# Optimization experiments

Hardware: AMD Instinct MI355X
Metric: run time of the kernel (lower is better)

The kernel has to match this reference:

```python
import jax, jax.numpy as jnp
import numpy as np

EPS = 1e-5
HEADS, K, U, M = 4, 16, 1, 11


def _bn(z, gamma, beta, mean, var):
    # z: [b, c, n]; BN in eval mode (running stats)
    inv = jax.lax.rsqrt(var + EPS)
    return (z - mean[None, :, None]) * (gamma * inv)[None, :, None] + beta[None, :, None]


def setup_inputs() -> dict:
    key = jax.random.key(0)
    ks = jax.random.split(key, 16)
    b, C, w, h = 8, 256, 64, 64
    vv = 256 // HEADS  # out_channels // heads = 64
    inp = {}
    inp['x'] = jax.random.normal(ks[0], (b, C, w, h), dtype=jnp.float32)
    sc = 1.0 / np.sqrt(C)
    inp['Wq'] = jax.random.normal(ks[1], (K * HEADS, C), dtype=jnp.float32) * sc
    inp['q_gamma'] = jnp.ones((K * HEADS,), jnp.float32)
    inp['q_beta'] = jnp.zeros((K * HEADS,), jnp.float32)
    inp['q_mean'] = jax.random.normal(ks[2], (K * HEADS,), dtype=jnp.float32) * 0.1
    inp['q_var'] = jax.random.uniform(ks[3], (K * HEADS,), minval=0.5, maxval=1.5, dtype=jnp.float32)
    inp['Wk'] = jax.random.normal(ks[4], (K * U, C), dtype=jnp.float32) * sc
    inp['Wv'] = jax.random.normal(ks[5], (vv * U, C), dtype=jnp.float32) * sc
    inp['v_gamma'] = jnp.ones((vv * U,), jnp.float32)
    inp['v_beta'] = jnp.zeros((vv * U,), jnp.float32)
    inp['v_mean'] = jax.random.normal(ks[6], (vv * U,), dtype=jnp.float32) * 0.1
    inp['v_var'] = jax.random.uniform(ks[7], (vv * U,), minval=0.5, maxval=1.5, dtype=jnp.float32)
    inp['embedding'] = jax.random.normal(ks[8], (K, U, 1, M, M), dtype=jnp.float32)
    return inp


def reference(x, Wq, q_gamma, q_beta, q_mean, q_var, Wk, Wv,
              v_gamma, v_beta, v_mean, v_var, embedding):
    b, C, w, h = x.shape
    n = w * h
    vv = Wv.shape[0] // U
    xf = x.reshape(b, C, n)

    # queries: 1x1 conv + BN -> [b, heads, k, n]
    q = _bn(jnp.einsum('oc,bcn->bon', Wq, xf), q_gamma, q_beta, q_mean, q_var)
    q = q.reshape(b, HEADS, K, n)

    # keys: 1x1 conv, softmax over spatial positions -> [b, k, u, n]
    keys = jnp.einsum('oc,bcn->bon', Wk, xf).reshape(b, K, U, n)
    sm = jax.nn.softmax(keys, axis=-1)

    # values: 1x1 conv + BN -> [b, vv, u, n]
    values = _bn(jnp.einsum('oc,bcn->bon', Wv, xf), v_gamma, v_beta, v_mean, v_var)
    values = values.reshape(b, vv, U, n)

    # content lambda
    lam_c = jnp.einsum('bkun,bvun->bkv', sm, values)          # [b, k, vv]
    y_c = jnp.einsum('bhkn,bkv->bhvn', q, lam_c)              # [b, h, vv, n]

    # position lambda via conv3d over (vv, w, h) with kernel (1, m, m)
    v5 = values.reshape(b, U, vv, w, h)                       # torch .view reinterpret
    pad = (M - 1) // 2
    lam_p = jax.lax.conv_general_dilated(
        v5, embedding, window_strides=(1, 1, 1),
        padding=((0, 0), (pad, pad), (pad, pad)),
        dimension_numbers=('NCDHW', 'OIDHW', 'NCDHW'))        # [b, k, vv, w, h]
    lam_p = lam_p.reshape(b, K, vv, n)
    y_p = jnp.einsum('bhkn,bkvn->bhvn', q, lam_p)             # [b, h, vv, n]

    out = (y_c + y_p).reshape(b, HEADS * vv, w, h)
    return out
```

## Files before the change

kernel.cpp:

```cpp
#include <hip/hip_runtime.h>
#include <math.h>

#define EPSBN 1e-5f

constexpr int B_ = 8, C_ = 256, N_ = 4096, IMG_ = 64;
constexpr int HEADS_ = 4, K_ = 16, VV_ = 64, M_ = 11, OC_ = 144;

typedef _Float16 half4 __attribute__((ext_vector_type(4)));
typedef _Float16 half8 __attribute__((ext_vector_type(8)));
typedef __fp16 fp16x2 __attribute__((ext_vector_type(2)));
typedef float f32x4 __attribute__((ext_vector_type(4)));

constexpr size_t O_WT   = 0;
constexpr size_t O_BIAS = 18432;
constexpr size_t O_EMBT = 18688;
constexpr size_t O_Q    = 24832;
constexpr size_t O_KEYS = O_Q    + 1048576;
constexpr size_t O_SINV = O_KEYS + 524288;
constexpr size_t O_VP   = 1597952;
constexpr size_t O_LC   = O_VP   + 1802240;

constexpr int VPROW = 88, VPPLANE = 80 * 88;

__global__ void k_prep(const float* __restrict__ Wq,
                       const float* __restrict__ qg, const float* __restrict__ qb,
                       const float* __restrict__ qm, const float* __restrict__ qv,
                       const float* __restrict__ Wk, const float* __restrict__ Wv,
                       const float* __restrict__ vg, const float* __restrict__ vb,
                       const float* __restrict__ vm, const float* __restrict__ vva,
                       const float* __restrict__ emb, float* __restrict__ ws) {
    int t = threadIdx.x, blk = blockIdx.x;
    if (blk >= 1776) {
        size_t i = (size_t)(blk - 1776) * 256 + t;
        f32x4 z = {0.f, 0.f, 0.f, 0.f};
        *(f32x4*)(ws + O_LC + i * 4) = z;
        return;
    }
    if (blk >= 16) {
        size_t i = (size_t)(blk - 16) * 256 + t;
        f32x4 z = {0.f, 0.f, 0.f, 0.f};
        *(f32x4*)(ws + O_VP + i * 4) = z;
        return;
    }
    _Float16* wf = (_Float16*)(ws + O_WT);
    int base = blk * 2304;
#pragma unroll
    for (int i = 0; i < 9; i++) {
        int idx = base + i * 256 + t;
        int o = idx >> 8, c = idx & 255;
        float w;
        if (o < 64) {
            float s = qg[o] * rsqrtf(qv[o] + EPSBN);
            w = Wq[o * 256 + c] * s;
        } else if (o < 80) {
            w = Wk[(o - 64) * 256 + c];
        } else {
            int ov = o - 80;
            float s = vg[ov] * rsqrtf(vva[ov] + EPSBN);
            w = Wv[ov * 256 + c] * s;
        }
        wf[idx] = (_Float16)w;
    }
    if (blk == 0 && t < 144) {
        float bias;
        if (t < 64) {
            float s = qg[t] * rsqrtf(qv[t] + EPSBN);
            bias = qb[t] - qm[t] * s;
        } else if (t < 80) {
            bias = 0.f;
        } else {
            int ov = t - 80;
            float s = vg[ov] * rsqrtf(vva[ov] + EPSBN);
            bias = vb[ov] - vm[ov] * s;
        }
        ws[O_BIAS + t] = bias;
    }
    if (blk == 15) {
        _Float16* ef = (_Float16*)(ws + O_EMBT);
        for (int idx = t; idx < 64 * 48; idx += 256) {
            int l = idx / 48, rem = idx % 48;
            int dp = rem >> 3, j = rem & 7;
            int k = l & 15, g = l >> 4;
            int dy = 2 * dp + (j >> 2);
            int dx = 4 * g + (j & 3);
            float v = (dy < 11 && dx < 11) ? emb[k * 121 + dy * 11 + dx] : 0.f;
            ef[idx] = (_Float16)v;
        }
    }
}

__global__ __launch_bounds__(256) void k_proj(const float* __restrict__ x,
                                              const float* __restrict__ wsc,
                                              float* __restrict__ ws) {
    __shared__ uint WL[144 * 68];
    __shared__ uint XL[64 * 68];
    int b    = blockIdx.y;
    int pos0 = blockIdx.x * 64;
    int t    = threadIdx.x;
    int w = t >> 6, l = t & 63;
    int g = l >> 4, r = l & 15;

    f32x4 acc[9];
#pragma unroll
    for (int mf = 0; mf < 9; mf++) acc[mf] = (f32x4){0.f, 0.f, 0.f, 0.f};

    const uint* wsrc = (const uint*)(wsc + O_WT);
    const float* xb = x + (size_t)b * C_ * N_ + pos0;
    union u4h { uint4 u; half8 h; };

    for (int kh = 0; kh < 2; kh++) {
        if (kh) __syncthreads();
#pragma unroll
        for (int i = 0; i < 9; i++) {
            int idx = t + i * 256;
            int o = idx >> 4, c4 = idx & 15;
            uint4 wv = *(const uint4*)(wsrc + o * 128 + kh * 64 + c4 * 4);
            *(uint4*)&WL[o * 68 + c4 * 4] = wv;
        }
#pragma unroll
        for (int i = 0; i < 4; i++) {
            int idx = t + i * 256;
            int cl = idx >> 4, p4 = idx & 15;
            float4 a0 = *(const float4*)(xb + (size_t)(2 * (64 * kh + cl)) * N_ + 4 * p4);
            float4 a1 = *(const float4*)(xb + (size_t)(2 * (64 * kh + cl) + 1) * N_ + 4 * p4);
            union { _Float16 h[2]; uint u; } pk;
#pragma unroll
            for (int j = 0; j < 4; j++) {
                float v0 = (j == 0) ? a0.x : (j == 1) ? a0.y : (j == 2) ? a0.z : a0.w;
                float v1 = (j == 0) ? a1.x : (j == 1) ? a1.y : (j == 2) ? a1.z : a1.w;
                pk.h[0] = (_Float16)v0; pk.h[1] = (_Float16)v1;
                XL[(4 * p4 + j) * 68 + cl] = pk.u;
            }
        }
        __syncthreads();

#pragma unroll
        for (int ks = 0; ks < 4; ks++) {
            int cu = 16 * ks + 4 * g;
            u4h bf;
            bf.u = *(const uint4*)&XL[(w * 16 + r) * 68 + cu];
#pragma unroll
            for (int mf = 0; mf < 9; mf++) {
                u4h af;
                af.u = *(const uint4*)&WL[(16 * mf + r) * 68 + cu];
                acc[mf] = __builtin_amdgcn_mfma_f32_16x16x32_f16(af.h, bf.h, acc[mf], 0, 0, 0);
            }
        }
    }

    int pos = pos0 + w * 16 + r;
#pragma unroll
    for (int mf = 0; mf < 9; mf++) {
        float4 bias4 = *(const float4*)(wsc + O_BIAS + 16 * mf + 4 * g);
        f32x4 a = acc[mf];
        float rv0 = a[0] + bias4.x, rv1 = a[1] + bias4.y;
        float rv2 = a[2] + bias4.z, rv3 = a[3] + bias4.w;
        if (mf < 4) {
            union { fp16x2 h[2]; uint2 u; } pk;
            pk.h[0] = __builtin_amdgcn_cvt_pkrtz(rv0, rv1);
            pk.h[1] = __builtin_amdgcn_cvt_pkrtz(rv2, rv3);
            ((uint2*)(ws + O_Q))[((size_t)(b * 16 + 4 * mf + g)) * N_ + pos] = pk.u;
        } else if (mf == 4) {
            int ch0 = 16 * mf + 4 * g;
            float* kp = ws + O_KEYS + ((size_t)(b * 16 + (ch0 - 64))) * N_ + pos;
            kp[0] = rv0; kp[(size_t)N_] = rv1; kp[2 * (size_t)N_] = rv2; kp[3 * (size_t)N_] = rv3;
        } else {
            int ov = 16 * mf + 4 * g - 80;
            int y = pos >> 6, xx = pos & 63;
            _Float16* vp = (_Float16*)(ws + O_VP) +
                           ((size_t)(b * 64 + ov)) * VPPLANE + (size_t)(y + 8) * VPROW + (xx + 8);
            vp[0] = (_Float16)rv0; vp[VPPLANE] = (_Float16)rv1;
            vp[2 * VPPLANE] = (_Float16)rv2; vp[3 * VPPLANE] = (_Float16)rv3;
        }
    }
}

__global__ __launch_bounds__(256) void k_ssum(float* __restrict__ ws) {
    int row = blockIdx.x;
    const float* src = ws + O_KEYS + (size_t)row * N_;
    int t = threadIdx.x;
    float s = 0.f;
#pragma unroll
    for (int i = 0; i < 4; i++) {
        float4 r = *(const float4*)(src + i * 1024 + t * 4);
        s += expf(r.x) + expf(r.y) + expf(r.z) + expf(r.w);
    }
    for (int off = 32; off > 0; off >>= 1) s += __shfl_xor(s, off);
    __shared__ float reds[4];
    if ((t & 63) == 0) reds[t >> 6] = s;
    __syncthreads();
    if (t == 0)
        ws[O_SINV + row] = 1.f / (reds[0] + reds[1] + reds[2] + reds[3]);
}

__global__ __launch_bounds__(256) void k_lamc(float* __restrict__ ws) {
    int b  = blockIdx.x >> 6;
    int ch = blockIdx.x & 63;
    int n0 = ch * 64;
    __shared__ float ek[16 * 64];
    int t = threadIdx.x;
    {
        int k = t >> 4, nq = t & 15;
        float4 kv = *(const float4*)(ws + O_KEYS + ((size_t)(b * 16 + k)) * N_ + n0 + 4 * nq);
        float is = ws[O_SINV + b * 16 + k];
        float4 e;
        e.x = expf(kv.x) * is; e.y = expf(kv.y) * is;
        e.z = expf(kv.z) * is; e.w = expf(kv.w) * is;
        *(float4*)&ek[k * 64 + 4 * nq] = e;
    }
    __syncthreads();

    int v  = t & 63;
    int kg = __builtin_amdgcn_readfirstlane(t >> 6);
    float acc[4] = {0.f, 0.f, 0.f, 0.f};
    const _Float16* vp = (const _Float16*)(ws + O_VP) +
                         (size_t)(b * 64 + v) * VPPLANE + (size_t)(ch + 8) * VPROW + 8;
    union U4 { uint4 q; _Float16 h[8]; } u[8];
#pragma unroll
    for (int iu = 0; iu < 8; iu++)
        u[iu].q = *(const uint4*)(vp + 8 * iu);
#pragma unroll
    for (int xq = 0; xq < 16; xq++) {
        float4 e0 = *(const float4*)&ek[(kg * 4 + 0) * 64 + 4 * xq];
        float4 e1 = *(const float4*)&ek[(kg * 4 + 1) * 64 + 4 * xq];
        float4 e2 = *(const float4*)&ek[(kg * 4 + 2) * 64 + 4 * xq];
        float4 e3 = *(const float4*)&ek[(kg * 4 + 3) * 64 + 4 * xq];
        float v0 = (float)u[xq >> 1].h[(xq & 1) * 4 + 0];
        float v1 = (float)u[xq >> 1].h[(xq & 1) * 4 + 1];
        float v2 = (float)u[xq >> 1].h[(xq & 1) * 4 + 2];
        float v3 = (float)u[xq >> 1].h[(xq & 1) * 4 + 3];
        acc[0] += e0.x * v0 + e0.y * v1 + e0.z * v2 + e0.w * v3;
        acc[1] += e1.x * v0 + e1.y * v1 + e1.z * v2 + e1.w * v3;
        acc[2] += e2.x * v0 + e2.y * v1 + e2.z * v2 + e2.w * v3;
        acc[3] += e3.x * v0 + e3.y * v1 + e3.z * v2 + e3.w * v3;
    }
#pragma unroll
    for (int j = 0; j < 4; j++)
        atomicAdd(ws + O_LC + ((size_t)(b * 16 + kg * 4 + j)) * 64 + v, acc[j]);
}

__global__ __launch_bounds__(256, 4) void k_out(const float* __restrict__ wsc,
                                                float* __restrict__ out) {
    __shared__ ushort vt[2][4][19][84];
    int ytile = blockIdx.x;
    int vc    = blockIdx.y;
    int b     = blockIdx.z;
    int y0 = ytile * 8, v0 = vc * 4;
    int t = threadIdx.x;
    int w = t >> 6, l = t & 63;
    int g = l >> 4, nb = l & 15;

    float4 lc4[4];
#pragma unroll
    for (int i = 0; i < 4; i++)
        lc4[i] = *(const float4*)(wsc + O_LC + ((size_t)(b * 16 + 4 * g + i)) * 64 + v0);

    union AF { uint4 u; half8 h; } af[6];
    {
        const uint4* ap = (const uint4*)((const _Float16*)(wsc + O_EMBT) + (size_t)l * 48);
#pragma unroll
        for (int dp = 0; dp < 6; dp++) af[dp].u = ap[dp];
    }

    const ushort* vpb = (const ushort*)(wsc + O_VP) + (size_t)(b * 64 + v0) * VPPLANE;
    for (int T = t; T < 1596; T += 256) {
        int v = T / 399, rem = T % 399;
        int r = rem / 21, qd = rem % 21;
        const ushort* src = vpb + (size_t)v * VPPLANE + (size_t)(y0 + 3 + r) * VPROW + 4 * qd;
        uint2 u01 = *(const uint2*)src;
        uint2 u23 = *(const uint2*)(src + 4);
        *(uint2*)&vt[0][v][r][4 * qd] = u01;
        uint lo = (u01.x >> 16) | (u01.y << 16);
        uint hi = (u01.y >> 16) | (u23.x << 16);
        *(uint2*)&vt[1][v][r][4 * qd] = make_uint2(lo, hi);
    }
    __syncthreads();

    const uint* vtu = (const uint*)&vt[0][0][0][0];
    const uint2* qfp = (const uint2*)(wsc + O_Q);

#pragma unroll
    for (int xt = 0; xt < 4; xt++) {
        int X = xt * 16 + nb;
        union QH { uint2 u; fp16x2 h[2]; } qh[2][4];
#pragma unroll
        for (int yy2 = 0; yy2 < 2; yy2++) {
            int pos = (y0 + 2 * w + yy2) * 64 + X;
#pragma unroll
            for (int j = 0; j < 4; j++)
                qh[yy2][j].u = qfp[((size_t)(b * 16 + 4 * (g ^ j) + g)) * N_ + pos];
        }
        int wcol = X + 4 * g + 3;
        int cp   = wcol & 1;
        int j0u  = (wcol - cp) >> 1;

#pragma unroll
        for (int v = 0; v < 4; v++) {
            int bwin = ((cp * 4 + v) * 19 + 2 * w) * 42 + j0u;
            uint2 win[13];
#pragma unroll
            for (int i = 0; i < 13; i++) {
                win[i].x = vtu[bwin + 42 * i];
                win[i].y = vtu[bwin + 42 * i + 1];
            }

#pragma unroll
            for (int yy2 = 0; yy2 < 2; yy2++) {
                f32x4 acc = {0.f, 0.f, 0.f, 0.f};
#pragma unroll
                for (int dp = 0; dp < 6; dp++) {
                    union { uint u[4]; half8 h; } bb;
                    bb.u[0] = win[yy2 + 2 * dp].x;
                    bb.u[1] = win[yy2 + 2 * dp].y;
                    bb.u[2] = win[yy2 + 2 * dp + 1].x;
                    bb.u[3] = win[yy2 + 2 * dp + 1].y;
                    acc = __builtin_amdgcn_mfma_f32_16x16x32_f16(af[dp].h, bb.h, acc, 0, 0, 0);
                }
                float d0 = acc[0] + lc4[0][v];
                float d1 = acc[1] + lc4[1][v];
                float d2 = acc[2] + lc4[2][v];
                float d3 = acc[3] + lc4[3][v];
                fp16x2 dlo = __builtin_amdgcn_cvt_pkrtz(d0, d1);
                fp16x2 dhi = __builtin_amdgcn_cvt_pkrtz(d2, d3);
                float ph[4];
#pragma unroll
                for (int j = 0; j < 4; j++)
                    ph[j] = __builtin_amdgcn_fdot2(qh[yy2][j].h[0], dlo,
                            __builtin_amdgcn_fdot2(qh[yy2][j].h[1], dhi, 0.f, false), false);
                float sa = ph[0] + __shfl_xor(ph[1], 16);
                float sb = ph[2] + __shfl_xor(ph[3], 16);
                float o  = sa + __shfl_xor(sb, 32);
                int pos = (y0 + 2 * w + yy2) * 64 + X;
                out[((size_t)(b * 256 + g * 64 + v0 + v)) * N_ + pos] = o;
            }
        }
    }
}

extern "C" void kernel_launch(void* const* d_in, const int* in_sizes, int n_in,
                              void* d_out, int out_size, void* d_ws, size_t ws_size,
                              hipStream_t stream) {
    const float* x   = (const float*)d_in[0];
    const float* Wq  = (const float*)d_in[1];
    const float* qg  = (const float*)d_in[2];
    const float* qb  = (const float*)d_in[3];
    const float* qm  = (const float*)d_in[4];
    const float* qv  = (const float*)d_in[5];
    const float* Wk  = (const float*)d_in[6];
    const float* Wv  = (const float*)d_in[7];
    const float* vg  = (const float*)d_in[8];
    const float* vb  = (const float*)d_in[9];
    const float* vm  = (const float*)d_in[10];
    const float* vva = (const float*)d_in[11];
    const float* emb = (const float*)d_in[12];
    float* ws  = (float*)d_ws;
    float* out = (float*)d_out;

    k_prep<<<1784, 256, 0, stream>>>(Wq, qg, qb, qm, qv, Wk, Wv, vg, vb, vm, vva, emb, ws);
    k_proj<<<dim3(64, 8), 256, 0, stream>>>(x, ws, ws);
    k_ssum<<<128, 256, 0, stream>>>(ws);
    k_lamc<<<512, 256, 0, stream>>>(ws);
    k_out<<<dim3(8, 16, 8), 256, 0, stream>>>(ws, out);
}
```

Baseline: 58.01 us.

## Fuse softmax denominator into lambda-content kernel and defer normalization

Removes the separate softmax-sum kernel. k_lamc now accumulates the unnormalized exp sums per key row with atomics while it computes exponentials, and k_out divides the content lambda by the sum when loading it. This saves one kernel launch and one extra pass over the keys buffer. In exchange it adds atomics on the sum buffer, and that buffer must be zeroed in k_prep.

```diff
diff --git a/kernel.cpp b/kernel.cpp
--- a/kernel.cpp
+++ b/kernel.cpp
@@ -61,19 +61,22 @@
         }
         wf[idx] = (_Float16)w;
     }
-    if (blk == 0 && t < 144) {
-        float bias;
-        if (t < 64) {
-            float s = qg[t] * rsqrtf(qv[t] + EPSBN);
-            bias = qb[t] - qm[t] * s;
-        } else if (t < 80) {
-            bias = 0.f;
-        } else {
-            int ov = t - 80;
-            float s = vg[ov] * rsqrtf(vva[ov] + EPSBN);
-            bias = vb[ov] - vm[ov] * s;
-        }
-        ws[O_BIAS + t] = bias;
+    if (blk == 0) {
+        if (t < 144) {
+            float bias;
+            if (t < 64) {
+                float s = qg[t] * rsqrtf(qv[t] + EPSBN);
+                bias = qb[t] - qm[t] * s;
+            } else if (t < 80) {
+                bias = 0.f;
+            } else {
+                int ov = t - 80;
+                float s = vg[ov] * rsqrtf(vva[ov] + EPSBN);
+                bias = vb[ov] - vm[ov] * s;
+            }
+            ws[O_BIAS + t] = bias;
+        }
+        if (t < 128) ws[O_SINV + t] = 0.f;
     }
     if (blk == 15) {
         _Float16* ef = (_Float16*)(ws + O_EMBT);
@@ -175,24 +178,6 @@
     }
 }
 
-__global__ __launch_bounds__(256) void k_ssum(float* __restrict__ ws) {
-    int row = blockIdx.x;
-    const float* src = ws + O_KEYS + (size_t)row * N_;
-    int t = threadIdx.x;
-    float s = 0.f;
-#pragma unroll
-    for (int i = 0; i < 4; i++) {
-        float4 r = *(const float4*)(src + i * 1024 + t * 4);
-        s += expf(r.x) + expf(r.y) + expf(r.z) + expf(r.w);
-    }
-    for (int off = 32; off > 0; off >>= 1) s += __shfl_xor(s, off);
-    __shared__ float reds[4];
-    if ((t & 63) == 0) reds[t >> 6] = s;
-    __syncthreads();
-    if (t == 0)
-        ws[O_SINV + row] = 1.f / (reds[0] + reds[1] + reds[2] + reds[3]);
-}
-
 __global__ __launch_bounds__(256) void k_lamc(float* __restrict__ ws) {
     int b  = blockIdx.x >> 6;
     int ch = blockIdx.x & 63;
@@ -202,11 +187,13 @@
     {
         int k = t >> 4, nq = t & 15;
         float4 kv = *(const float4*)(ws + O_KEYS + ((size_t)(b * 16 + k)) * N_ + n0 + 4 * nq);
-        float is = ws[O_SINV + b * 16 + k];
         float4 e;
-        e.x = expf(kv.x) * is; e.y = expf(kv.y) * is;
-        e.z = expf(kv.z) * is; e.w = expf(kv.w) * is;
+        e.x = expf(kv.x); e.y = expf(kv.y); e.z = expf(kv.z); e.w = expf(kv.w);
         *(float4*)&ek[k * 64 + 4 * nq] = e;
+        float s = e.x + e.y + e.z + e.w;
+#pragma unroll
+        for (int off = 1; off < 16; off <<= 1) s += __shfl_xor(s, off);
+        if (nq == 0) atomicAdd(ws + O_SINV + b * 16 + k, s);
     }
     __syncthreads();
 
@@ -251,9 +238,15 @@
     int g = l >> 4, nb = l & 15;
 
     float4 lc4[4];
-#pragma unroll
-    for (int i = 0; i < 4; i++)
-        lc4[i] = *(const float4*)(wsc + O_LC + ((size_t)(b * 16 + 4 * g + i)) * 64 + v0);
+    float4 ssum4 = *(const float4*)(wsc + O_SINV + b * 16 + 4 * g);
+#pragma unroll
+    for (int i = 0; i < 4; i++) {
+        float inv = 1.f / ((i == 0) ? ssum4.x : (i == 1) ? ssum4.y
+                          : (i == 2) ? ssum4.z : ssum4.w);
+        float4 lv = *(const float4*)(wsc + O_LC + ((size_t)(b * 16 + 4 * g + i)) * 64 + v0);
+        lv.x *= inv; lv.y *= inv; lv.z *= inv; lv.w *= inv;
+        lc4[i] = lv;
+    }
 
     union AF { uint4 u; half8 h; } af[6];
     {
@@ -358,7 +351,6 @@
 
     k_prep<<<1784, 256, 0, stream>>>(Wq, qg, qb, qm, qv, Wk, Wv, vg, vb, vm, vva, emb, ws);
     k_proj<<<dim3(64, 8), 256, 0, stream>>>(x, ws, ws);
-    k_ssum<<<128, 256, 0, stream>>>(ws);
     k_lamc<<<512, 256, 0, stream>>>(ws);
     k_out<<<dim3(8, 16, 8), 256, 0, stream>>>(ws, out);
 }
```

Measured after the change: 60.09 us. 3.6% more time.
